# Kernel tuning notes

Hardware: AMD Instinct MI355X
Metric: run time of the kernel (lower is better)

Reference implementation:

```python
import jax, jax.numpy as jnp
import numpy as np

B, S, D = 4, 1024, 1024
E, F, TOPK = 16, 512, 4


def setup_inputs() -> dict:
    key = jax.random.key(0)
    k1, k2, k3, k4, k5 = jax.random.split(key, 5)
    scale = 0.02
    return {
        "x": jax.random.normal(k1, (B, S, D), dtype=jnp.float32),
        "Wr": jax.random.normal(k2, (D, E), dtype=jnp.float32) * scale,   # router
        "Wg": jax.random.normal(k3, (E, D, F), dtype=jnp.float32) * scale,  # gate proj
        "Wu": jax.random.normal(k4, (E, D, F), dtype=jnp.float32) * scale,  # up proj
        "Wd": jax.random.normal(k5, (E, F, D), dtype=jnp.float32) * scale,  # down proj
    }


def reference(x, Wr, Wg, Wu, Wd):
    b, s, d = x.shape
    xf = x.reshape(-1, d)                      # [N, D], N = B*S
    n = xf.shape[0]
    e = Wr.shape[1]

    # --- router: softmax over experts, top-k, renormalized weights ---
    probs = jax.nn.softmax(xf @ Wr, axis=-1)   # [N, E]
    w, idx = jax.lax.top_k(probs, TOPK)        # [N, K], [N, K]
    w = w / jnp.sum(w, axis=-1, keepdims=True)

    # combine weights per (token, expert); zero for unselected experts.
    # Equivalent to the per-expert where/gather/scatter-add loop in torch.
    cw = jnp.zeros((n, e), dtype=xf.dtype).at[jnp.arange(n)[:, None], idx].add(w)

    # --- per-expert gated FFN (SwiGLU), combined with routing weights ---
    def body(acc, ws):
        wg, wu, wd, c = ws                     # [D,F], [D,F], [F,D], [N]
        h = jax.nn.silu(xf @ wg) * (xf @ wu)   # [N, F]
        return acc + c[:, None] * (h @ wd), None

    out, _ = jax.lax.scan(body, jnp.zeros_like(xf), (Wg, Wu, Wd, cw.T))
    return out.reshape(b, s, d)
```

## Files before the change

### kernel.cpp

```cpp
#include <hip/hip_runtime.h>

#define N_TOK 4096
#define DIM   1024
#define NE    16
#define NF    512
#define TOPK  4
#define CAP   4096
#define NPAIR (N_TOK * TOPK)
#define MAXTILES 144
#define GU_BLOCKS (4 * MAXTILES)
#define DN_BLOCKS (4 * MAXTILES)
#define PREPD_BLOCKS (NE * 128)
#define RP_ROUTER 1024
#define RP_PREP   4096

typedef _Float16 v8h __attribute__((ext_vector_type(8)));
typedef float    v4f __attribute__((ext_vector_type(4)));

__device__ __forceinline__ void prep_tile256(
    const float* __restrict__ src, unsigned short* __restrict__ dst,
    int R, int C, int RIL, int e, int cbl, int rbl, float (*tile)[65])
{
    int c0 = cbl * 64, r0 = rbl * 64;
    const float* s = src + (size_t)e * R * C;
    int t = threadIdx.x;
    int tr = t >> 4, tc = (t & 15) * 4;
#pragma unroll
    for (int i = 0; i < 4; i++) {
        int row = i * 16 + tr;
        float4 v = *(const float4*)(s + (size_t)(r0 + row) * C + c0 + tc);
        tile[row][tc + 0] = v.x; tile[row][tc + 1] = v.y;
        tile[row][tc + 2] = v.z; tile[row][tc + 3] = v.w;
    }
    __syncthreads();
    int ktPerE = R >> 5;
    int cbPerE = C >> RIL;
    int imgSz  = (1 << RIL) * 32;
#pragma unroll
    for (int i = 0; i < 4; i++) {
        int nr = i * 16 + tr;
        int orow = c0 + nr;
        int k0 = r0 + tc;
        int cb = orow >> RIL;
        int r  = orow & ((1 << RIL) - 1);
        int kt = k0 >> 5;
        size_t off = ((size_t)(e * cbPerE + cb) * ktPerE + kt) * imgSz
                   + r * 32 + (k0 & 31);
        union { unsigned short u[4]; uint2 v; } p;
#pragma unroll
        for (int j = 0; j < 4; j++)
            p.u[j] = __builtin_bit_cast(unsigned short, (_Float16)tile[tc + j][nr]);
        *(uint2*)(dst + off) = p.v;
    }
}

__device__ __forceinline__ void prep_tile512(
    const float* __restrict__ src, unsigned short* __restrict__ dst,
    int R, int C, int RIL, int e, int cbl, int rbl, float (*tile)[65])
{
    int c0 = cbl * 64, r0 = rbl * 64;
    const float* s = src + (size_t)e * R * C;
    int t = threadIdx.x;
    int tr = t >> 4;
    int tc = (t & 15) * 4;
#pragma unroll
    for (int i = 0; i < 2; i++) {
        int row = i * 32 + tr;
        float4 v = *(const float4*)(s + (size_t)(r0 + row) * C + c0 + tc);
        tile[row][tc + 0] = v.x; tile[row][tc + 1] = v.y;
        tile[row][tc + 2] = v.z; tile[row][tc + 3] = v.w;
    }
    __syncthreads();
    int ktPerE = R >> 5;
    int cbPerE = C >> RIL;
    int imgSz  = (1 << RIL) * 32;
#pragma unroll
    for (int i = 0; i < 2; i++) {
        int nr = i * 32 + tr;
        int orow = c0 + nr;
        int k0 = r0 + tc;
        int cb = orow >> RIL;
        int r  = orow & ((1 << RIL) - 1);
        int kt = k0 >> 5;
        size_t off = ((size_t)(e * cbPerE + cb) * ktPerE + kt) * imgSz
                   + r * 32 + (k0 & 31);
        union { unsigned short u[4]; uint2 v; } p;
#pragma unroll
        for (int j = 0; j < 4; j++)
            p.u[j] = __builtin_bit_cast(unsigned short, (_Float16)tile[tc + j][nr]);
        *(uint2*)(dst + off) = p.v;
    }
}

__global__ __launch_bounds__(256) void router_prep_kernel(
    const float* __restrict__ x, const float* __restrict__ Wr,
    const float* __restrict__ Wg, const float* __restrict__ Wu,
    int* __restrict__ tokIdx, float* __restrict__ tokW,
    unsigned short* __restrict__ xb,
    unsigned short* __restrict__ Wg_t, unsigned short* __restrict__ Wu_t)
{
    __shared__ __align__(16) float tile[64][65];
    int bid = blockIdx.x;
    if (bid >= RP_ROUTER) {
        int pid = bid - RP_ROUTER;
        int z = pid >> 7;
        int which = z >> 4, e = z & 15;
        int bx = pid & 127;
        int cbl = bx & 7, rbl = bx >> 3;
        prep_tile256(which ? Wu : Wg, which ? Wu_t : Wg_t,
                     DIM, NF, 6, e, cbl, rbl, tile);
        return;
    }
    int tid = threadIdx.x;
    int w = tid >> 6, l = tid & 63;
    int t = bid * 4 + w;

    double z[NE];
#pragma unroll
    for (int e = 0; e < NE; e++) z[e] = 0.0;
    const float* xrow = x + (size_t)t * DIM;
#pragma unroll
    for (int i = 0; i < 16; i++) {
        int d = i * 64 + l;
        double xv = (double)xrow[d];
        const float4* wr = (const float4*)(Wr + d * NE);
        float4 w0 = wr[0], w1 = wr[1], w2 = wr[2], w3 = wr[3];
        z[0]  += xv * w0.x; z[1]  += xv * w0.y; z[2]  += xv * w0.z; z[3]  += xv * w0.w;
        z[4]  += xv * w1.x; z[5]  += xv * w1.y; z[6]  += xv * w1.z; z[7]  += xv * w1.w;
        z[8]  += xv * w2.x; z[9]  += xv * w2.y; z[10] += xv * w2.z; z[11] += xv * w2.w;
        z[12] += xv * w3.x; z[13] += xv * w3.y; z[14] += xv * w3.z; z[15] += xv * w3.w;
    }
    const float4* xv4 = (const float4*)xrow;
#pragma unroll
    for (int h2 = 0; h2 < 2; h2++) {
        int base = h2 * 512 + l * 8;
        float4 a = xv4[h2 * 128 + l * 2];
        float4 b = xv4[h2 * 128 + l * 2 + 1];
        union { unsigned short u[8]; uint4 v; } p;
        p.u[0] = __builtin_bit_cast(unsigned short, (_Float16)a.x);
        p.u[1] = __builtin_bit_cast(unsigned short, (_Float16)a.y);
        p.u[2] = __builtin_bit_cast(unsigned short, (_Float16)a.z);
        p.u[3] = __builtin_bit_cast(unsigned short, (_Float16)a.w);
        p.u[4] = __builtin_bit_cast(unsigned short, (_Float16)b.x);
        p.u[5] = __builtin_bit_cast(unsigned short, (_Float16)b.y);
        p.u[6] = __builtin_bit_cast(unsigned short, (_Float16)b.z);
        p.u[7] = __builtin_bit_cast(unsigned short, (_Float16)b.w);
        *(uint4*)(xb + (size_t)t * DIM + base) = p.v;
    }
#pragma unroll
    for (int e = 0; e < NE; e++) {
#pragma unroll
        for (int m = 1; m < 64; m <<= 1) z[e] += __shfl_xor(z[e], m, 64);
    }
    if (l == 0) {
        bool taken[NE];
#pragma unroll
        for (int e = 0; e < NE; e++) taken[e] = false;
        int idx[TOPK]; double sel[TOPK];
        for (int k = 0; k < TOPK; k++) {
            int bi = 0; double bv = -1.0e300;
            for (int e = 0; e < NE; e++)
                if (!taken[e] && z[e] > bv) { bv = z[e]; bi = e; }
            taken[bi] = true; idx[k] = bi; sel[k] = bv;
        }
        double m = sel[0];
        double ex[TOPK]; double s = 0.0;
        for (int k = 0; k < TOPK; k++) { ex[k] = exp(sel[k] - m); s += ex[k]; }
        for (int k = 0; k < TOPK; k++) {
            tokIdx[t * TOPK + k] = idx[k];
            tokW[t * TOPK + k]   = (float)(ex[k] / s);
        }
    }
}

__global__ __launch_bounds__(256) void bin_kernel(
    const int* __restrict__ tokIdx,
    int* __restrict__ cnt, int* __restrict__ bpair)
{
    int e = blockIdx.x;
    int tid = threadIdx.x, lane = tid & 63, wv = tid >> 6;
    __shared__ int wsum[4];
    __shared__ int sbase;
    if (tid == 0) sbase = 0;
    __syncthreads();
    unsigned long long lt = (1ULL << lane) - 1ULL;
#pragma unroll 1
    for (int c0 = 0; c0 < NPAIR; c0 += 1024) {
        int i0 = c0 + tid * 4;
        int4 v = *(const int4*)(tokIdx + i0);
        int m[4] = {v.x == e, v.y == e, v.z == e, v.w == e};
        int r[4]; int wcnt = 0;
#pragma unroll
        for (int j = 0; j < 4; j++) {
            unsigned long long bal = __ballot(m[j] != 0);
            r[j] = wcnt + __popcll(bal & lt);
            wcnt += __popcll(bal);
        }
        if (lane == 0) wsum[wv] = wcnt;
        __syncthreads();
        int woff = sbase;
        for (int k = 0; k < wv; k++) woff += wsum[k];
#pragma unroll
        for (int j = 0; j < 4; j++)
            if (m[j]) bpair[e * CAP + woff + r[j]] = i0 + j;
        __syncthreads();
        if (tid == 0) sbase += wsum[0] + wsum[1] + wsum[2] + wsum[3];
        __syncthreads();
    }
    if (tid == 0) cnt[e] = sbase;
}

__device__ __forceinline__ int ldsw(int row, int chunk) {
    return row * 32 + (chunk ^ ((row >> 1) & 3)) * 8;
}

__device__ __forceinline__ void gload16(const unsigned short* g, unsigned short* l) {
    __builtin_amdgcn_global_load_lds(
        (const __attribute__((address_space(1))) void*)g,
        (__attribute__((address_space(3))) void*)l, 16, 0, 0);
}

__device__ __forceinline__ bool find_tile(const int* __restrict__ cnt,
                                          int ti, int& e, int& mt, int& tbase) {
    int rt = 0;
#pragma unroll 1
    for (int ee = 0; ee < NE; ee++) {
        int nt = (cnt[ee] + 127) >> 7;
        if (ti < rt + nt) { e = ee; mt = ti - rt; tbase = rt; return true; }
        rt += nt;
    }
    return false;
}

__global__ __launch_bounds__(512, 4) void ffn_gate_up_kernel(
    const unsigned short* __restrict__ xb,
    const unsigned short* __restrict__ Wg_t,
    const unsigned short* __restrict__ Wu_t,
    const int* __restrict__ cnt,
    const int* __restrict__ bpair,
    unsigned short* __restrict__ h_t,
    const float* __restrict__ Wd,
    unsigned short* __restrict__ Wd_t)
{
    __shared__ __align__(16) unsigned char smem[49664];
    unsigned short* sX = (unsigned short*)smem;
    unsigned short* sG = (unsigned short*)(smem + 16384);
    unsigned short* sU = (unsigned short*)(smem + 32768);
    int* sTok = (int*)(smem + 49152);
    float (*tile)[65] = (float (*)[65])smem;

    int bid = blockIdx.x;
    if (bid >= GU_BLOCKS) {
        int pid = bid - GU_BLOCKS;
        int e = pid >> 7;
        int bx = pid & 127;
        int cbl = bx & 15, rbl = bx >> 4;
        prep_tile512(Wd, Wd_t, NF, DIM, 7, e, cbl, rbl, tile);
        return;
    }
    int fb = bid & 3, ti = bid >> 2;
    int e, mt, tbase;
    if (!find_tile(cnt, ti, e, mt, tbase)) return;
    int count = cnt[e];

    int tid = threadIdx.x, lane = tid & 63, w = tid >> 6;
    if (tid < 128) {
        int pos = mt * 128 + tid;
        sTok[tid] = bpair[e * CAP + min(pos, count - 1)] >> 2;
    }
    __syncthreads();

    int srow = tid >> 2;
    int spos = tid & 3;
    int cx = spos ^ ((srow >> 1) & 3);
    const unsigned short* gX = xb + (size_t)sTok[srow] * DIM + cx * 8;
    const unsigned short* gG = Wg_t
        + ((size_t)(e * 8 + fb * 2 + (srow >> 6)) * 32) * 2048
        + (srow & 63) * 32 + cx * 8;
    const unsigned short* gU = Wu_t
        + ((size_t)(e * 8 + fb * 2 + (srow >> 6)) * 32) * 2048
        + (srow & 63) * 32 + cx * 8;
    unsigned short* dX = sX + w * 512;
    unsigned short* dG = sG + w * 512;
    unsigned short* dU = sU + w * 512;

    int row = lane & 15, q = lane >> 4;
    int rw = w & 1, cw = w >> 1;
    int aoff[4], goff[2];
#pragma unroll
    for (int mi = 0; mi < 4; mi++) aoff[mi] = ldsw(rw * 64 + mi * 16 + row, q);
#pragma unroll
    for (int ni = 0; ni < 2; ni++) goff[ni] = ldsw(cw * 32 + ni * 16 + row, q);

    v4f accG[4][2], accU[4][2];
    v4f zero = {0.f, 0.f, 0.f, 0.f};
#pragma unroll
    for (int mi = 0; mi < 4; mi++)
#pragma unroll
        for (int ni = 0; ni < 2; ni++) { accG[mi][ni] = zero; accU[mi][ni] = zero; }

#define STAGE_GU(b, kt) do {                                   \
        gload16(gX + (kt) * 32, dX + (b) * 4096);              \
        gload16(gG + (size_t)(kt) * 2048, dG + (b) * 4096);    \
        gload16(gU + (size_t)(kt) * 2048, dU + (b) * 4096);    \
    } while (0)

    STAGE_GU(0, 0);

#pragma unroll 1
    for (int kt = 0; kt < 32; kt++) {
        int buf = kt & 1;
        if (kt < 31) {
            STAGE_GU(buf ^ 1, kt + 1);
            asm volatile("s_waitcnt vmcnt(3)" ::: "memory");
        } else {
            asm volatile("s_waitcnt vmcnt(0)" ::: "memory");
        }
        __builtin_amdgcn_s_barrier();
        __builtin_amdgcn_sched_barrier(0);
        const unsigned short* bX = sX + buf * 4096;
        const unsigned short* bGp = sG + buf * 4096;
        const unsigned short* bUp = sU + buf * 4096;
        v8h a[4], bg[2], bu[2];
#pragma unroll
        for (int mi = 0; mi < 4; mi++) a[mi] = *(const v8h*)&bX[aoff[mi]];
#pragma unroll
        for (int ni = 0; ni < 2; ni++) {
            bg[ni] = *(const v8h*)&bGp[goff[ni]];
            bu[ni] = *(const v8h*)&bUp[goff[ni]];
        }
#pragma unroll
        for (int mi = 0; mi < 4; mi++)
#pragma unroll
            for (int ni = 0; ni < 2; ni++) {
                accG[mi][ni] = __builtin_amdgcn_mfma_f32_16x16x32_f16(a[mi], bg[ni], accG[mi][ni], 0, 0, 0);
                accU[mi][ni] = __builtin_amdgcn_mfma_f32_16x16x32_f16(a[mi], bu[ni], accU[mi][ni], 0, 0, 0);
            }
        __builtin_amdgcn_sched_barrier(0);
        __builtin_amdgcn_s_barrier();
        __builtin_amdgcn_sched_barrier(0);
    }
#undef STAGE_GU

    size_t himg = (size_t)(tbase + mt) * 16;
#pragma unroll
    for (int mi = 0; mi < 4; mi++)
#pragma unroll
        for (int ni = 0; ni < 2; ni++) {
            int f = fb * 128 + cw * 32 + ni * 16 + row;
#pragma unroll
            for (int i = 0; i < 4; i++) {
                int rl = rw * 64 + mi * 16 + q * 4 + i;
                int pos = mt * 128 + rl;
                if (pos < count) {
                    float gv = accG[mi][ni][i];
                    float uv = accU[mi][ni][i];
                    float hv = gv * uv / (1.0f + __expf(-gv));
                    size_t off = (himg + (f >> 5)) * 4096 + rl * 32 + (f & 31);
                    h_t[off] = __builtin_bit_cast(unsigned short, (_Float16)hv);
                }
            }
        }
}

__global__ __launch_bounds__(512, 4) void ffn_down_kernel(
    const unsigned short* __restrict__ h_t,
    const unsigned short* __restrict__ Wd_t,
    const int* __restrict__ cnt,
    const int* __restrict__ bpair,
    unsigned short* __restrict__ part)
{
    __shared__ __align__(16) unsigned short sH[2 * 128 * 32];
    __shared__ __align__(16) unsigned short sW[2 * 256 * 32];
    __shared__ int sPair[128];

    int bid = blockIdx.x;
    int db = bid & 3, ti = bid >> 2;
    int e, mt, tbase;
    if (!find_tile(cnt, ti, e, mt, tbase)) return;
    int count = cnt[e];

    int tid = threadIdx.x, lane = tid & 63, w = tid >> 6;
    if (tid < 128) {
        int pos = mt * 128 + tid;
        sPair[tid] = bpair[e * CAP + min(pos, count - 1)];
    }
    __syncthreads();

    int srow = tid >> 2;
    int spos = tid & 3;
    int cx = spos ^ ((srow >> 1) & 3);
    const unsigned short* gH = h_t + ((size_t)(tbase + mt) * 16) * 4096
                             + srow * 32 + cx * 8;
    const unsigned short* gW0 = Wd_t + ((size_t)(e * 8 + db * 2 + 0) * 16) * 4096
                              + srow * 32 + cx * 8;
    const unsigned short* gW1 = Wd_t + ((size_t)(e * 8 + db * 2 + 1) * 16) * 4096
                              + srow * 32 + cx * 8;
    unsigned short* dH  = sH + w * 512;
    unsigned short* dW0 = sW + w * 512;
    unsigned short* dW1 = sW + 4096 + w * 512;

    int row = lane & 15, q = lane >> 4;
    int rw = w & 1, cw = w >> 1;
    int aoff[4], boff[4];
#pragma unroll
    for (int mi = 0; mi < 4; mi++) aoff[mi] = ldsw(rw * 64 + mi * 16 + row, q);
#pragma unroll
    for (int ni = 0; ni < 4; ni++) boff[ni] = ldsw(cw * 64 + ni * 16 + row, q);

    v4f acc[4][4];
    v4f zero = {0.f, 0.f, 0.f, 0.f};
#pragma unroll
    for (int mi = 0; mi < 4; mi++)
#pragma unroll
        for (int ni = 0; ni < 4; ni++) acc[mi][ni] = zero;

#define STAGE_D(b, kt) do {                                         \
        gload16(gH + (size_t)(kt) * 4096, dH + (b) * 4096);         \
        gload16(gW0 + (size_t)(kt) * 4096, dW0 + (b) * 8192);       \
        gload16(gW1 + (size_t)(kt) * 4096, dW1 + (b) * 8192);       \
    } while (0)

    STAGE_D(0, 0);

#pragma unroll 1
    for (int kt = 0; kt < 16; kt++) {
        int buf = kt & 1;
        if (kt < 15) {
            STAGE_D(buf ^ 1, kt + 1);
            asm volatile("s_waitcnt vmcnt(3)" ::: "memory");
        } else {
            asm volatile("s_waitcnt vmcnt(0)" ::: "memory");
        }
        __builtin_amdgcn_s_barrier();
        __builtin_amdgcn_sched_barrier(0);
        const unsigned short* bH = sH + buf * 4096;
        const unsigned short* bW = sW + buf * 8192;
        v8h a[4], b[4];
#pragma unroll
        for (int mi = 0; mi < 4; mi++) a[mi] = *(const v8h*)&bH[aoff[mi]];
#pragma unroll
        for (int ni = 0; ni < 4; ni++) b[ni] = *(const v8h*)&bW[boff[ni]];
#pragma unroll
        for (int mi = 0; mi < 4; mi++)
#pragma unroll
            for (int ni = 0; ni < 4; ni++)
                acc[mi][ni] = __builtin_amdgcn_mfma_f32_16x16x32_f16(a[mi], b[ni], acc[mi][ni], 0, 0, 0);
        __builtin_amdgcn_sched_barrier(0);
        __builtin_amdgcn_s_barrier();
        __builtin_amdgcn_sched_barrier(0);
    }
#undef STAGE_D

#pragma unroll
    for (int mi = 0; mi < 4; mi++)
#pragma unroll
        for (int ni = 0; ni < 4; ni++) {
            int col = db * 256 + cw * 64 + ni * 16 + row;
#pragma unroll
            for (int i = 0; i < 4; i++) {
                int rl = rw * 64 + mi * 16 + q * 4 + i;
                int pos = mt * 128 + rl;
                if (pos < count) {
                    int p = sPair[rl];
                    part[(size_t)p * DIM + col] =
                        __builtin_bit_cast(unsigned short, (_Float16)acc[mi][ni][i]);
                }
            }
        }
}

__global__ __launch_bounds__(256) void combine_kernel(
    const unsigned short* __restrict__ part, const float* __restrict__ tokW,
    float* __restrict__ out)
{
    int gid = blockIdx.x * 256 + threadIdx.x;
    int t = gid >> 8;
    int c = (gid & 255) * 4;
    float4 r = {0.f, 0.f, 0.f, 0.f};
#pragma unroll
    for (int k = 0; k < TOPK; k++) {
        float wk = tokW[t * TOPK + k];
        union { uint2 u; _Float16 h[4]; } cv;
        cv.u = *(const uint2*)(part + ((size_t)(t * TOPK + k)) * DIM + c);
        r.x += wk * (float)cv.h[0];
        r.y += wk * (float)cv.h[1];
        r.z += wk * (float)cv.h[2];
        r.w += wk * (float)cv.h[3];
    }
    *(float4*)(out + (size_t)t * DIM + c) = r;
}

extern "C" void kernel_launch(void* const* d_in, const int* in_sizes, int n_in,
                              void* d_out, int out_size, void* d_ws, size_t ws_size,
                              hipStream_t stream)
{
    const float* x  = (const float*)d_in[0];
    const float* Wr = (const float*)d_in[1];
    const float* Wg = (const float*)d_in[2];
    const float* Wu = (const float*)d_in[3];
    const float* Wd = (const float*)d_in[4];
    float* out = (float*)d_out;
    char* ws = (char*)d_ws;

    size_t off = 0;
    int* tokIdx = (int*)(ws + off);   off += (size_t)NPAIR * 4;
    float* tokW = (float*)(ws + off); off += (size_t)NPAIR * 4;
    int* cnt    = (int*)(ws + off);   off += 256;
    int* bpair  = (int*)(ws + off);   off += (size_t)NE * CAP * 4;
    unsigned short* xb   = (unsigned short*)(ws + off); off += (size_t)N_TOK * DIM * 2;
    unsigned short* Wg_t = (unsigned short*)(ws + off); off += (size_t)NE * DIM * NF * 2;
    unsigned short* Wu_t = (unsigned short*)(ws + off); off += (size_t)NE * DIM * NF * 2;
    unsigned short* Wd_t = (unsigned short*)(ws + off); off += (size_t)NE * DIM * NF * 2;
    unsigned short* h_t  = (unsigned short*)(ws + off); off += (size_t)MAXTILES * 16 * 4096 * 2;
    unsigned short* part = (unsigned short*)(ws + off); off += (size_t)NPAIR * DIM * 2;

    router_prep_kernel<<<RP_ROUTER + RP_PREP, 256, 0, stream>>>(
        x, Wr, Wg, Wu, tokIdx, tokW, xb, Wg_t, Wu_t);
    bin_kernel<<<NE, 256, 0, stream>>>(tokIdx, cnt, bpair);
    ffn_gate_up_kernel<<<GU_BLOCKS + PREPD_BLOCKS, 512, 0, stream>>>(
        xb, Wg_t, Wu_t, cnt, bpair, h_t, Wd, Wd_t);
    ffn_down_kernel<<<DN_BLOCKS, 512, 0, stream>>>(
        h_t, Wd_t, cnt, bpair, part);
    combine_kernel<<<(N_TOK * DIM) / (256 * 4), 256, 0, stream>>>(part, tokW, out);
}
```

Measured before the change: 275.7 us.

## Halve block size in FFN GEMMs and double per-wave output tile

The gate/up and down GEMM kernels drop from 512 to 256 threads per block while keeping the same block tile. Each wave now computes twice as many output columns (4x4 and 4x8 MFMA accumulators) and issues twice as many async global-to-LDS loads per stage. This raises the MFMA-to-LDS-read ratio per wave. In exchange it costs more accumulator registers and lowers occupancy, and the Wd prep path switches to the 256-thread tile helper.

```diff
diff --git a/kernel.cpp b/kernel.cpp
--- a/kernel.cpp
+++ b/kernel.cpp
@@ -39,44 +39,6 @@
 #pragma unroll
     for (int i = 0; i < 4; i++) {
         int nr = i * 16 + tr;
-        int orow = c0 + nr;
-        int k0 = r0 + tc;
-        int cb = orow >> RIL;
-        int r  = orow & ((1 << RIL) - 1);
-        int kt = k0 >> 5;
-        size_t off = ((size_t)(e * cbPerE + cb) * ktPerE + kt) * imgSz
-                   + r * 32 + (k0 & 31);
-        union { unsigned short u[4]; uint2 v; } p;
-#pragma unroll
-        for (int j = 0; j < 4; j++)
-            p.u[j] = __builtin_bit_cast(unsigned short, (_Float16)tile[tc + j][nr]);
-        *(uint2*)(dst + off) = p.v;
-    }
-}
-
-__device__ __forceinline__ void prep_tile512(
-    const float* __restrict__ src, unsigned short* __restrict__ dst,
-    int R, int C, int RIL, int e, int cbl, int rbl, float (*tile)[65])
-{
-    int c0 = cbl * 64, r0 = rbl * 64;
-    const float* s = src + (size_t)e * R * C;
-    int t = threadIdx.x;
-    int tr = t >> 4;
-    int tc = (t & 15) * 4;
-#pragma unroll
-    for (int i = 0; i < 2; i++) {
-        int row = i * 32 + tr;
-        float4 v = *(const float4*)(s + (size_t)(r0 + row) * C + c0 + tc);
-        tile[row][tc + 0] = v.x; tile[row][tc + 1] = v.y;
-        tile[row][tc + 2] = v.z; tile[row][tc + 3] = v.w;
-    }
-    __syncthreads();
-    int ktPerE = R >> 5;
-    int cbPerE = C >> RIL;
-    int imgSz  = (1 << RIL) * 32;
-#pragma unroll
-    for (int i = 0; i < 2; i++) {
-        int nr = i * 32 + tr;
         int orow = c0 + nr;
         int k0 = r0 + tc;
         int cb = orow >> RIL;
@@ -232,7 +194,7 @@
     return false;
 }
 
-__global__ __launch_bounds__(512, 4) void ffn_gate_up_kernel(
+__global__ __launch_bounds__(256, 2) void ffn_gate_up_kernel(
     const unsigned short* __restrict__ xb,
     const unsigned short* __restrict__ Wg_t,
     const unsigned short* __restrict__ Wu_t,
@@ -255,7 +217,7 @@
         int e = pid >> 7;
         int bx = pid & 127;
         int cbl = bx & 15, rbl = bx >> 4;
-        prep_tile512(Wd, Wd_t, NF, DIM, 7, e, cbl, rbl, tile);
+        prep_tile256(Wd, Wd_t, NF, DIM, 7, e, cbl, rbl, tile);
         return;
     }
     int fb = bid & 3, ti = bid >> 2;
@@ -273,36 +235,41 @@
     int srow = tid >> 2;
     int spos = tid & 3;
     int cx = spos ^ ((srow >> 1) & 3);
-    const unsigned short* gX = xb + (size_t)sTok[srow] * DIM + cx * 8;
-    const unsigned short* gG = Wg_t
-        + ((size_t)(e * 8 + fb * 2 + (srow >> 6)) * 32) * 2048
-        + (srow & 63) * 32 + cx * 8;
-    const unsigned short* gU = Wu_t
-        + ((size_t)(e * 8 + fb * 2 + (srow >> 6)) * 32) * 2048
-        + (srow & 63) * 32 + cx * 8;
-    unsigned short* dX = sX + w * 512;
-    unsigned short* dG = sG + w * 512;
-    unsigned short* dU = sU + w * 512;
+    const unsigned short* gX0 = xb + (size_t)sTok[srow] * DIM + cx * 8;
+    const unsigned short* gX1 = xb + (size_t)sTok[srow + 64] * DIM + cx * 8;
+    const unsigned short* gG0 = Wg_t + ((size_t)(e * 8 + fb * 2 + 0) * 32) * 2048 + srow * 32 + cx * 8;
+    const unsigned short* gG1 = Wg_t + ((size_t)(e * 8 + fb * 2 + 1) * 32) * 2048 + srow * 32 + cx * 8;
+    const unsigned short* gU0 = Wu_t + ((size_t)(e * 8 + fb * 2 + 0) * 32) * 2048 + srow * 32 + cx * 8;
+    const unsigned short* gU1 = Wu_t + ((size_t)(e * 8 + fb * 2 + 1) * 32) * 2048 + srow * 32 + cx * 8;
+    unsigned short* dX0 = sX + w * 512;
+    unsigned short* dX1 = sX + 2048 + w * 512;
+    unsigned short* dG0 = sG + w * 512;
+    unsigned short* dG1 = sG + 2048 + w * 512;
+    unsigned short* dU0 = sU + w * 512;
+    unsigned short* dU1 = sU + 2048 + w * 512;
 
     int row = lane & 15, q = lane >> 4;
     int rw = w & 1, cw = w >> 1;
-    int aoff[4], goff[2];
+    int aoff[4], goff[4];
 #pragma unroll
     for (int mi = 0; mi < 4; mi++) aoff[mi] = ldsw(rw * 64 + mi * 16 + row, q);
 #pragma unroll
-    for (int ni = 0; ni < 2; ni++) goff[ni] = ldsw(cw * 32 + ni * 16 + row, q);
-
-    v4f accG[4][2], accU[4][2];
+    for (int ni = 0; ni < 4; ni++) goff[ni] = ldsw(cw * 64 + ni * 16 + row, q);
+
+    v4f accG[4][4], accU[4][4];
     v4f zero = {0.f, 0.f, 0.f, 0.f};
 #pragma unroll
     for (int mi = 0; mi < 4; mi++)
 #pragma unroll
-        for (int ni = 0; ni < 2; ni++) { accG[mi][ni] = zero; accU[mi][ni] = zero; }
-
-#define STAGE_GU(b, kt) do {                                   \
-        gload16(gX + (kt) * 32, dX + (b) * 4096);              \
-        gload16(gG + (size_t)(kt) * 2048, dG + (b) * 4096);    \
-        gload16(gU + (size_t)(kt) * 2048, dU + (b) * 4096);    \
+        for (int ni = 0; ni < 4; ni++) { accG[mi][ni] = zero; accU[mi][ni] = zero; }
+
+#define STAGE_GU(b, kt) do {                                       \
+        gload16(gX0 + (kt) * 32, dX0 + (b) * 4096);                \
+        gload16(gX1 + (kt) * 32, dX1 + (b) * 4096);                \
+        gload16(gG0 + (size_t)(kt) * 2048, dG0 + (b) * 4096);      \
+        gload16(gG1 + (size_t)(kt) * 2048, dG1 + (b) * 4096);      \
+        gload16(gU0 + (size_t)(kt) * 2048, dU0 + (b) * 4096);      \
+        gload16(gU1 + (size_t)(kt) * 2048, dU1 + (b) * 4096);      \
     } while (0)
 
     STAGE_GU(0, 0);
@@ -312,7 +279,7 @@
         int buf = kt & 1;
         if (kt < 31) {
             STAGE_GU(buf ^ 1, kt + 1);
-            asm volatile("s_waitcnt vmcnt(3)" ::: "memory");
+            asm volatile("s_waitcnt vmcnt(6)" ::: "memory");
         } else {
             asm volatile("s_waitcnt vmcnt(0)" ::: "memory");
         }
@@ -321,18 +288,18 @@
         const unsigned short* bX = sX + buf * 4096;
         const unsigned short* bGp = sG + buf * 4096;
         const unsigned short* bUp = sU + buf * 4096;
-        v8h a[4], bg[2], bu[2];
+        v8h a[4], bg[4], bu[4];
 #pragma unroll
         for (int mi = 0; mi < 4; mi++) a[mi] = *(const v8h*)&bX[aoff[mi]];
 #pragma unroll
-        for (int ni = 0; ni < 2; ni++) {
+        for (int ni = 0; ni < 4; ni++) {
             bg[ni] = *(const v8h*)&bGp[goff[ni]];
             bu[ni] = *(const v8h*)&bUp[goff[ni]];
         }
 #pragma unroll
         for (int mi = 0; mi < 4; mi++)
 #pragma unroll
-            for (int ni = 0; ni < 2; ni++) {
+            for (int ni = 0; ni < 4; ni++) {
                 accG[mi][ni] = __builtin_amdgcn_mfma_f32_16x16x32_f16(a[mi], bg[ni], accG[mi][ni], 0, 0, 0);
                 accU[mi][ni] = __builtin_amdgcn_mfma_f32_16x16x32_f16(a[mi], bu[ni], accU[mi][ni], 0, 0, 0);
             }
@@ -346,8 +313,8 @@
 #pragma unroll
     for (int mi = 0; mi < 4; mi++)
 #pragma unroll
-        for (int ni = 0; ni < 2; ni++) {
-            int f = fb * 128 + cw * 32 + ni * 16 + row;
+        for (int ni = 0; ni < 4; ni++) {
+            int f = fb * 128 + cw * 64 + ni * 16 + row;
 #pragma unroll
             for (int i = 0; i < 4; i++) {
                 int rl = rw * 64 + mi * 16 + q * 4 + i;
@@ -363,7 +330,7 @@
         }
 }
 
-__global__ __launch_bounds__(512, 4) void ffn_down_kernel(
+__global__ __launch_bounds__(256, 2) void ffn_down_kernel(
     const unsigned short* __restrict__ h_t,
     const unsigned short* __restrict__ Wd_t,
     const int* __restrict__ cnt,
@@ -390,35 +357,44 @@
     int srow = tid >> 2;
     int spos = tid & 3;
     int cx = spos ^ ((srow >> 1) & 3);
-    const unsigned short* gH = h_t + ((size_t)(tbase + mt) * 16) * 4096
-                             + srow * 32 + cx * 8;
-    const unsigned short* gW0 = Wd_t + ((size_t)(e * 8 + db * 2 + 0) * 16) * 4096
-                              + srow * 32 + cx * 8;
-    const unsigned short* gW1 = Wd_t + ((size_t)(e * 8 + db * 2 + 1) * 16) * 4096
-                              + srow * 32 + cx * 8;
-    unsigned short* dH  = sH + w * 512;
+    const unsigned short* hbase = h_t + ((size_t)(tbase + mt) * 16) * 4096;
+    const unsigned short* gH0 = hbase + srow * 32 + cx * 8;
+    const unsigned short* gH1 = hbase + (srow + 64) * 32 + cx * 8;
+    const unsigned short* w0base = Wd_t + ((size_t)(e * 8 + db * 2 + 0) * 16) * 4096;
+    const unsigned short* w1base = Wd_t + ((size_t)(e * 8 + db * 2 + 1) * 16) * 4096;
+    const unsigned short* gW0 = w0base + srow * 32 + cx * 8;
+    const unsigned short* gW1 = w0base + (srow + 64) * 32 + cx * 8;
+    const unsigned short* gW2 = w1base + srow * 32 + cx * 8;
+    const unsigned short* gW3 = w1base + (srow + 64) * 32 + cx * 8;
+    unsigned short* dH0 = sH + w * 512;
+    unsigned short* dH1 = sH + 2048 + w * 512;
     unsigned short* dW0 = sW + w * 512;
-    unsigned short* dW1 = sW + 4096 + w * 512;
+    unsigned short* dW1 = sW + 2048 + w * 512;
+    unsigned short* dW2 = sW + 4096 + w * 512;
+    unsigned short* dW3 = sW + 6144 + w * 512;
 
     int row = lane & 15, q = lane >> 4;
     int rw = w & 1, cw = w >> 1;
-    int aoff[4], boff[4];
+    int aoff[4], boff[8];
 #pragma unroll
     for (int mi = 0; mi < 4; mi++) aoff[mi] = ldsw(rw * 64 + mi * 16 + row, q);
 #pragma unroll
-    for (int ni = 0; ni < 4; ni++) boff[ni] = ldsw(cw * 64 + ni * 16 + row, q);
-
-    v4f acc[4][4];
+    for (int ni = 0; ni < 8; ni++) boff[ni] = ldsw(cw * 128 + ni * 16 + row, q);
+
+    v4f acc[4][8];
     v4f zero = {0.f, 0.f, 0.f, 0.f};
 #pragma unroll
     for (int mi = 0; mi < 4; mi++)
 #pragma unroll
-        for (int ni = 0; ni < 4; ni++) acc[mi][ni] = zero;
+        for (int ni = 0; ni < 8; ni++) acc[mi][ni] = zero;
 
 #define STAGE_D(b, kt) do {                                         \
-        gload16(gH + (size_t)(kt) * 4096, dH + (b) * 4096);         \
+        gload16(gH0 + (size_t)(kt) * 4096, dH0 + (b) * 4096);       \
+        gload16(gH1 + (size_t)(kt) * 4096, dH1 + (b) * 4096);       \
         gload16(gW0 + (size_t)(kt) * 4096, dW0 + (b) * 8192);       \
         gload16(gW1 + (size_t)(kt) * 4096, dW1 + (b) * 8192);       \
+        gload16(gW2 + (size_t)(kt) * 4096, dW2 + (b) * 8192);       \
+        gload16(gW3 + (size_t)(kt) * 4096, dW3 + (b) * 8192);       \
     } while (0)
 
     STAGE_D(0, 0);
@@ -428,7 +404,7 @@
         int buf = kt & 1;
         if (kt < 15) {
             STAGE_D(buf ^ 1, kt + 1);
-            asm volatile("s_waitcnt vmcnt(3)" ::: "memory");
+            asm volatile("s_waitcnt vmcnt(6)" ::: "memory");
         } else {
             asm volatile("s_waitcnt vmcnt(0)" ::: "memory");
         }
@@ -436,15 +412,15 @@
         __builtin_amdgcn_sched_barrier(0);
         const unsigned short* bH = sH + buf * 4096;
         const unsigned short* bW = sW + buf * 8192;
-        v8h a[4], b[4];
+        v8h a[4], b[8];
 #pragma unroll
         for (int mi = 0; mi < 4; mi++) a[mi] = *(const v8h*)&bH[aoff[mi]];
 #pragma unroll
-        for (int ni = 0; ni < 4; ni++) b[ni] = *(const v8h*)&bW[boff[ni]];
+        for (int ni = 0; ni < 8; ni++) b[ni] = *(const v8h*)&bW[boff[ni]];
 #pragma unroll
         for (int mi = 0; mi < 4; mi++)
 #pragma unroll
-            for (int ni = 0; ni < 4; ni++)
+            for (int ni = 0; ni < 8; ni++)
                 acc[mi][ni] = __builtin_amdgcn_mfma_f32_16x16x32_f16(a[mi], b[ni], acc[mi][ni], 0, 0, 0);
         __builtin_amdgcn_sched_barrier(0);
         __builtin_amdgcn_s_barrier();
@@ -455,8 +431,8 @@
 #pragma unroll
     for (int mi = 0; mi < 4; mi++)
 #pragma unroll
-        for (int ni = 0; ni < 4; ni++) {
-            int col = db * 256 + cw * 64 + ni * 16 + row;
+        for (int ni = 0; ni < 8; ni++) {
+            int col = db * 256 + cw * 128 + ni * 16 + row;
 #pragma unroll
             for (int i = 0; i < 4; i++) {
                 int rl = rw * 64 + mi * 16 + q * 4 + i;
@@ -518,9 +494,9 @@
     router_prep_kernel<<<RP_ROUTER + RP_PREP, 256, 0, stream>>>(
         x, Wr, Wg, Wu, tokIdx, tokW, xb, Wg_t, Wu_t);
     bin_kernel<<<NE, 256, 0, stream>>>(tokIdx, cnt, bpair);
-    ffn_gate_up_kernel<<<GU_BLOCKS + PREPD_BLOCKS, 512, 0, stream>>>(
+    ffn_gate_up_kernel<<<GU_BLOCKS + PREPD_BLOCKS, 256, 0, stream>>>(
         xb, Wg_t, Wu_t, cnt, bpair, h_t, Wd, Wd_t);
-    ffn_down_kernel<<<DN_BLOCKS, 512, 0, stream>>>(
+    ffn_down_kernel<<<DN_BLOCKS, 256, 0, stream>>>(
         h_t, Wd_t, cnt, bpair, part);
     combine_kernel<<<(N_TOK * DIM) / (256 * 4), 256, 0, stream>>>(part, tokW, out);
 }
```

Result: slower. 283.9 us (+3.0%).
